# Optimization experiments

Measured on AMD Instinct MI355X. Metric: run time of the kernel, lower is better.

The kernel has to match this reference:

```python
import jax, jax.numpy as jnp
import numpy as np

EPS = 1e-5

def _layernorm(x, g, b):
    mu = jnp.mean(x, axis=-1, keepdims=True)
    var = jnp.mean(jnp.square(x - mu), axis=-1, keepdims=True)
    return (x - mu) * jax.lax.rsqrt(var + EPS) * g + b

def setup_inputs() -> dict:
    key = jax.random.key(0)
    ks = jax.random.split(key, 6)
    B, S, D, F = 32768, 8, 192, 384
    sd = 1.0 / np.sqrt(D)
    return {
        "x": jax.random.normal(ks[0], (B, S, D), jnp.float32),
        "w_qkv": jax.random.normal(ks[1], (D, 3 * D), jnp.float32) * sd,
        "w_out": jax.random.normal(ks[2], (D, D), jnp.float32) * sd,
        "b_out": jnp.zeros((D,), jnp.float32),
        "g1": jnp.ones((D,), jnp.float32),
        "b1": jnp.zeros((D,), jnp.float32),
        "g2": jnp.ones((D,), jnp.float32),
        "b2": jnp.zeros((D,), jnp.float32),
        "w_f1": jax.random.normal(ks[3], (D, F), jnp.float32) * sd,
        "b_f1": jnp.zeros((F,), jnp.float32),
        "w_f2": jax.random.normal(ks[4], (F, D), jnp.float32) * (1.0 / np.sqrt(F)),
        "b_f2": jnp.zeros((D,), jnp.float32),
    }

def reference(x, w_qkv, w_out, b_out, g1, b1, g2, b2, w_f1, b_f1, w_f2, b_f2):
    B, S, D = x.shape
    H = 4
    DH = D // H
    scale = DH ** -0.5
    normed = _layernorm(x, g1, b1)
    qkv = jnp.einsum('bsd,de->bse', normed, w_qkv)  # (B,S,3D)
    q, k, v = jnp.split(qkv, 3, axis=-1)
    q = q.reshape(B, S, H, DH)
    k = k.reshape(B, S, H, DH)
    v = v.reshape(B, S, H, DH)
    attn = jnp.einsum('bqhd,bkhd->bhqk', q, k) * scale
    attn = jax.nn.softmax(attn, axis=-1)
    out = jnp.einsum('bhqk,bkhd->bqhd', attn, v).reshape(B, S, D)
    out = jnp.einsum('bsd,de->bse', out, w_out) + b_out
    x = x + out
    h = _layernorm(x, g2, b2)
    h = jax.nn.gelu(jnp.einsum('bsd,df->bsf', h, w_f1) + b_f1, approximate=False)
    h = jnp.einsum('bsf,fd->bsd', h, w_f2) + b_f2
    return x + h
```

## Files before the change

kernel.cpp:

```cpp
#include <hip/hip_runtime.h>
#include <hip/hip_bf16.h>

typedef __bf16 bf16x8 __attribute__((ext_vector_type(8)));
typedef float f32x4 __attribute__((ext_vector_type(4)));

#define DEV static __device__ __forceinline__

DEV unsigned short f2b(float f) {
  return __builtin_bit_cast(unsigned short, __float2bfloat16(f));
}
DEV unsigned pk2(float a, float b) {
  return (unsigned)f2b(a) | ((unsigned)f2b(b) << 16);
}
DEV void unpack2(unsigned u, float& lo, float& hi) {
  lo = __uint_as_float(u << 16);
  hi = __uint_as_float(u & 0xffff0000u);
}
DEV float gelu_fast(float h) {
  float u = h * (1.5957691216f + 0.0713554f * h * h);
  float e = __expf(u);
  float r = __builtin_amdgcn_rcpf(e + 1.f);
  return h - h * r;
}

__global__ void pack_weights(const float* __restrict__ wq,
                             const float* __restrict__ wo,
                             const float* __restrict__ wf1,
                             const float* __restrict__ wf2,
                             unsigned short* __restrict__ ws) {
  int i = blockIdx.x * 256 + threadIdx.x;
  const float* src; int j, N, KC;
  if (i < 110592)      { j = i;          src = wq;  N = 576; KC = 6; }
  else if (i < 147456) { j = i - 110592; src = wo;  N = 192; KC = 6; }
  else if (i < 221184) { j = i - 147456; src = wf1; N = 384; KC = 6; }
  else                 { j = i - 221184; src = wf2; N = 192; KC = 12; }
  int tk = j >> 9, r = j & 511;
  int nt = tk / KC, kc = tk % KC;
  int n = nt * 16 + (r >> 5), k = kc * 32 + (r & 31);
  ws[i] = f2b(src[k * N + n]);
}

template<int NT, int KC, typename EPI>
DEV void gemm_stage(const unsigned short* As, int astride,
                    const unsigned short* Bp, int nt0, int KCtot,
                    int lr, int kg, EPI epi) {
  bf16x8 af[2][KC];
  #pragma unroll
  for (int m = 0; m < 2; ++m)
    #pragma unroll
    for (int kc = 0; kc < KC; ++kc)
      af[m][kc] = *(const bf16x8*)(As + (m * 16 + lr) * astride + kc * 32 + kg * 8);
  const unsigned short* bb = Bp + lr * 32 + kg * 8;
  bf16x8 bbuf[2][KC];
  #pragma unroll
  for (int kc = 0; kc < KC; ++kc)
    bbuf[0][kc] = *(const bf16x8*)(bb + (size_t)(nt0 * KCtot + kc) * 512);
  #pragma unroll
  for (int nt = 0; nt < NT; ++nt) {
    if (nt + 1 < NT) {
      #pragma unroll
      for (int kc = 0; kc < KC; ++kc)
        bbuf[(nt + 1) & 1][kc] =
            *(const bf16x8*)(bb + (size_t)((nt0 + nt + 1) * KCtot + kc) * 512);
    }
    f32x4 acc[2] = {};
    #pragma unroll
    for (int kc = 0; kc < KC; ++kc)
      #pragma unroll
      for (int m = 0; m < 2; ++m)
        acc[m] = __builtin_amdgcn_mfma_f32_16x16x32_bf16(bbuf[nt & 1][kc], af[m][kc], acc[m], 0, 0, 0);
    epi(nt, acc);
  }
}

template<bool ADD_A>
DEV void layernorm_pass(const float* __restrict__ xg, const unsigned short* Abuf,
                        unsigned short* dst,
                        const float* __restrict__ gg, const float* __restrict__ bb,
                        int t) {
  int r = t >> 3, q = t & 7;
  float vals[24];
  float s = 0.f;
  #pragma unroll
  for (int j = 0; j < 6; ++j) {
    float4 v = *(const float4*)(xg + (size_t)r * 192 + q * 24 + j * 4);
    if (ADD_A) {
      uint2 a2 = *(const uint2*)(Abuf + r * 392 + 192 + q * 24 + j * 4);
      float a0, a1, a2f, a3;
      unpack2(a2.x, a0, a1); unpack2(a2.y, a2f, a3);
      v.x += a0; v.y += a1; v.z += a2f; v.w += a3;
    }
    vals[j*4+0] = v.x; vals[j*4+1] = v.y; vals[j*4+2] = v.z; vals[j*4+3] = v.w;
    s += v.x + v.y + v.z + v.w;
  }
  s += __shfl_xor(s, 1); s += __shfl_xor(s, 2); s += __shfl_xor(s, 4);
  float mu = s * (1.f / 192.f);
  float ss = 0.f;
  #pragma unroll
  for (int i = 0; i < 24; ++i) { float d = vals[i] - mu; ss += d * d; }
  ss += __shfl_xor(ss, 1); ss += __shfl_xor(ss, 2); ss += __shfl_xor(ss, 4);
  float rstd = rsqrtf(ss * (1.f / 192.f) + 1e-5f);
  #pragma unroll
  for (int j = 0; j < 6; ++j) {
    int c = q * 24 + j * 4;
    float4 g4 = *(const float4*)(gg + c);
    float4 b4 = *(const float4*)(bb + c);
    uint2 u;
    u.x = pk2((vals[j*4+0] - mu) * rstd * g4.x + b4.x,
              (vals[j*4+1] - mu) * rstd * g4.y + b4.y);
    u.y = pk2((vals[j*4+2] - mu) * rstd * g4.z + b4.z,
              (vals[j*4+3] - mu) * rstd * g4.w + b4.w);
    *(uint2*)(dst + r * 200 + c) = u;
  }
}

__global__ __launch_bounds__(256, 3)
void fused_block(const float* __restrict__ x,
                 const float* __restrict__ g1, const float* __restrict__ b1,
                 const float* __restrict__ g2, const float* __restrict__ b2,
                 const float* __restrict__ b_out, const float* __restrict__ b_f1,
                 const float* __restrict__ b_f2,
                 const unsigned short* __restrict__ wq_t,
                 const unsigned short* __restrict__ wo_t,
                 const unsigned short* __restrict__ wf1_t,
                 const unsigned short* __restrict__ wf2_t,
                 float* __restrict__ out)
{
  __shared__ __align__(16) unsigned short r1[32 * 200];
  __shared__ __align__(16) unsigned short r2[32 * 392];

  const int t = threadIdx.x;
  const int wave = t >> 6;
  const int lane = t & 63;
  const int lr = lane & 15;
  const int kg = lane >> 4;
  const int token0 = blockIdx.x * 32;
  const float* xg = x + (size_t)token0 * 192;
  float* og = out + (size_t)token0 * 192;

  layernorm_pass<false>(xg, nullptr, r1, g1, b1, t);
  __syncthreads();

  gemm_stage<6, 6>(r1, 200, wq_t, wave * 6, 6, lr, kg,
    [&](int nt, f32x4 (&acc)[2]) {
      int n0 = (wave * 6 + nt) * 16 + kg * 4;
      #pragma unroll
      for (int m = 0; m < 2; ++m) {
        uint2 u; u.x = pk2(acc[m][0], acc[m][1]); u.y = pk2(acc[m][2], acc[m][3]);
        *(uint2*)(r2 + (m * 16 + lr) * 392 + n0) = u;
      }
    });
  __syncthreads();

  const int ag = t >> 4, aqi = (t >> 1) & 7, ahalf = t & 1;
  const int abl = ag >> 2, ah = ag & 3;
  const int aqrow = abl * 8 + aqi;
  const int ad0 = ahalf * 24;
  float p[8];
  {
    float qv[24];
    const uint4* qp = (const uint4*)(r2 + aqrow * 392 + ah * 48 + ad0);
    #pragma unroll
    for (int u = 0; u < 3; ++u) {
      uint4 w4 = qp[u];
      unpack2(w4.x, qv[u*8+0], qv[u*8+1]);
      unpack2(w4.y, qv[u*8+2], qv[u*8+3]);
      unpack2(w4.z, qv[u*8+4], qv[u*8+5]);
      unpack2(w4.w, qv[u*8+6], qv[u*8+7]);
    }
    #pragma unroll
    for (int j = 0; j < 8; ++j) {
      const uint4* kp = (const uint4*)(r2 + (abl * 8 + j) * 392 + 192 + ah * 48 + ad0);
      float d = 0.f;
      #pragma unroll
      for (int u = 0; u < 3; ++u) {
        uint4 w4 = kp[u];
        float lo, hi;
        unpack2(w4.x, lo, hi); d = fmaf(lo, qv[u*8+0], d); d = fmaf(hi, qv[u*8+1], d);
        unpack2(w4.y, lo, hi); d = fmaf(lo, qv[u*8+2], d); d = fmaf(hi, qv[u*8+3], d);
        unpack2(w4.z, lo, hi); d = fmaf(lo, qv[u*8+4], d); d = fmaf(hi, qv[u*8+5], d);
        unpack2(w4.w, lo, hi); d = fmaf(lo, qv[u*8+6], d); d = fmaf(hi, qv[u*8+7], d);
      }
      d += __shfl_xor(d, 1);
      p[j] = d * 0.14433756729740643f;
    }
    float mx = p[0];
    #pragma unroll
    for (int j = 1; j < 8; ++j) mx = fmaxf(mx, p[j]);
    float sum = 0.f;
    #pragma unroll
    for (int j = 0; j < 8; ++j) { p[j] = __expf(p[j] - mx); sum += p[j]; }
    float inv = 1.f / sum;
    #pragma unroll
    for (int j = 0; j < 8; ++j) p[j] *= inv;
  }
  __syncthreads();

  gemm_stage<3, 6>(r1, 200, wq_t, 24 + wave * 3, 6, lr, kg,
    [&](int nt, f32x4 (&acc)[2]) {
      int n0 = (wave * 3 + nt) * 16 + kg * 4;
      #pragma unroll
      for (int m = 0; m < 2; ++m) {
        uint2 u; u.x = pk2(acc[m][0], acc[m][1]); u.y = pk2(acc[m][2], acc[m][3]);
        *(uint2*)(r2 + (m * 16 + lr) * 392 + n0) = u;
      }
    });
  __syncthreads();

  {
    float oa[24];
    #pragma unroll
    for (int e = 0; e < 24; ++e) oa[e] = 0.f;
    #pragma unroll
    for (int j = 0; j < 8; ++j) {
      float pj = p[j];
      const uint4* vp = (const uint4*)(r2 + (abl * 8 + j) * 392 + ah * 48 + ad0);
      #pragma unroll
      for (int u = 0; u < 3; ++u) {
        uint4 w4 = vp[u];
        float lo, hi;
        unpack2(w4.x, lo, hi); oa[u*8+0] = fmaf(pj, lo, oa[u*8+0]); oa[u*8+1] = fmaf(pj, hi, oa[u*8+1]);
        unpack2(w4.y, lo, hi); oa[u*8+2] = fmaf(pj, lo, oa[u*8+2]); oa[u*8+3] = fmaf(pj, hi, oa[u*8+3]);
        unpack2(w4.z, lo, hi); oa[u*8+4] = fmaf(pj, lo, oa[u*8+4]); oa[u*8+5] = fmaf(pj, hi, oa[u*8+5]);
        unpack2(w4.w, lo, hi); oa[u*8+6] = fmaf(pj, lo, oa[u*8+6]); oa[u*8+7] = fmaf(pj, hi, oa[u*8+7]);
      }
    }
    uint4 ov[3];
    #pragma unroll
    for (int u = 0; u < 3; ++u) {
      ov[u].x = pk2(oa[u*8+0], oa[u*8+1]);
      ov[u].y = pk2(oa[u*8+2], oa[u*8+3]);
      ov[u].z = pk2(oa[u*8+4], oa[u*8+5]);
      ov[u].w = pk2(oa[u*8+6], oa[u*8+7]);
    }
    uint4* op = (uint4*)(r1 + aqrow * 200 + ah * 48 + ad0);
    #pragma unroll
    for (int u = 0; u < 3; ++u) op[u] = ov[u];
  }
  __syncthreads();

  uint2 areg[3][2];
  gemm_stage<3, 6>(r1, 200, wo_t, wave * 3, 6, lr, kg,
    [&](int nt, f32x4 (&acc)[2]) {
      int n0 = (wave * 3 + nt) * 16 + kg * 4;
      float4 bo = *(const float4*)(b_out + n0);
      #pragma unroll
      for (int m = 0; m < 2; ++m) {
        uint2 u;
        u.x = pk2(acc[m][0] + bo.x, acc[m][1] + bo.y);
        u.y = pk2(acc[m][2] + bo.z, acc[m][3] + bo.w);
        areg[nt][m] = u;
        *(uint2*)(r2 + (m * 16 + lr) * 392 + 192 + n0) = u;
      }
    });
  __syncthreads();

  layernorm_pass<true>(xg, r2, r1, g2, b2, t);
  __syncthreads();

  gemm_stage<6, 6>(r1, 200, wf1_t, wave * 6, 6, lr, kg,
    [&](int nt, f32x4 (&acc)[2]) {
      int n0 = (wave * 6 + nt) * 16 + kg * 4;
      float4 bf = *(const float4*)(b_f1 + n0);
      #pragma unroll
      for (int m = 0; m < 2; ++m) {
        float ge[4];
        #pragma unroll
        for (int i = 0; i < 4; ++i)
          ge[i] = gelu_fast(acc[m][i] + ((const float*)&bf)[i]);
        uint2 u; u.x = pk2(ge[0], ge[1]); u.y = pk2(ge[2], ge[3]);
        *(uint2*)(r2 + (m * 16 + lr) * 392 + n0) = u;
      }
    });
  __syncthreads();

  {
    f32x4 acc[3][2] = {};
    bf16x8 afb[2][2], bvb[2][3];
    #pragma unroll
    for (int m = 0; m < 2; ++m)
      afb[0][m] = *(const bf16x8*)(r2 + (m * 16 + lr) * 392 + kg * 8);
    #pragma unroll
    for (int nt = 0; nt < 3; ++nt)
      bvb[0][nt] = *(const bf16x8*)(wf2_t + (size_t)((wave * 3 + nt) * 12) * 512 + lr * 32 + kg * 8);
    #pragma unroll
    for (int kc = 0; kc < 12; ++kc) {
      if (kc + 1 < 12) {
        #pragma unroll
        for (int m = 0; m < 2; ++m)
          afb[(kc + 1) & 1][m] =
              *(const bf16x8*)(r2 + (m * 16 + lr) * 392 + (kc + 1) * 32 + kg * 8);
        #pragma unroll
        for (int nt = 0; nt < 3; ++nt)
          bvb[(kc + 1) & 1][nt] =
              *(const bf16x8*)(wf2_t + (size_t)((wave * 3 + nt) * 12 + kc + 1) * 512 + lr * 32 + kg * 8);
      }
      #pragma unroll
      for (int nt = 0; nt < 3; ++nt)
        #pragma unroll
        for (int m = 0; m < 2; ++m)
          acc[nt][m] = __builtin_amdgcn_mfma_f32_16x16x32_bf16(bvb[kc & 1][nt], afb[kc & 1][m], acc[nt][m], 0, 0, 0);
    }
    #pragma unroll
    for (int nt = 0; nt < 3; ++nt) {
      int n0 = (wave * 3 + nt) * 16 + kg * 4;
      float4 bf = *(const float4*)(b_f2 + n0);
      #pragma unroll
      for (int m = 0; m < 2; ++m) {
        int row = m * 16 + lr;
        float4 xv = *(const float4*)(xg + (size_t)row * 192 + n0);
        float a0, a1, a2f, a3;
        unpack2(areg[nt][m].x, a0, a1); unpack2(areg[nt][m].y, a2f, a3);
        float4 o;
        o.x = xv.x + a0  + acc[nt][m][0] + bf.x;
        o.y = xv.y + a1  + acc[nt][m][1] + bf.y;
        o.z = xv.z + a2f + acc[nt][m][2] + bf.z;
        o.w = xv.w + a3  + acc[nt][m][3] + bf.w;
        *(float4*)(og + (size_t)row * 192 + n0) = o;
      }
    }
  }
}

extern "C" void kernel_launch(void* const* d_in, const int* in_sizes, int n_in,
                              void* d_out, int out_size, void* d_ws, size_t ws_size,
                              hipStream_t stream) {
  const float* x   = (const float*)d_in[0];
  const float* wq  = (const float*)d_in[1];
  const float* wo  = (const float*)d_in[2];
  const float* bo  = (const float*)d_in[3];
  const float* g1  = (const float*)d_in[4];
  const float* b1  = (const float*)d_in[5];
  const float* g2  = (const float*)d_in[6];
  const float* b2  = (const float*)d_in[7];
  const float* wf1 = (const float*)d_in[8];
  const float* bf1 = (const float*)d_in[9];
  const float* wf2 = (const float*)d_in[10];
  const float* bf2 = (const float*)d_in[11];
  unsigned short* wsb = (unsigned short*)d_ws;

  pack_weights<<<1152, 256, 0, stream>>>(wq, wo, wf1, wf2, wsb);

  int tokens = in_sizes[0] / 192;
  int nb = tokens / 32;
  fused_block<<<nb, 256, 0, stream>>>(x, g1, b1, g2, b2, bo, bf1, bf2,
      wsb, wsb + 110592, wsb + 147456, wsb + 221184, (float*)d_out);
}
```

Before: 376.6 us.

## Prefetch weight tiles and x rows before barriers; use native bf16 pack

```diff
diff --git a/kernel.cpp b/kernel.cpp
--- a/kernel.cpp
+++ b/kernel.cpp
@@ -2,15 +2,18 @@
 #include <hip/hip_bf16.h>
 
 typedef __bf16 bf16x8 __attribute__((ext_vector_type(8)));
+typedef __bf16 bf16x2 __attribute__((ext_vector_type(2)));
 typedef float f32x4 __attribute__((ext_vector_type(4)));
 
 #define DEV static __device__ __forceinline__
 
 DEV unsigned short f2b(float f) {
-  return __builtin_bit_cast(unsigned short, __float2bfloat16(f));
+  __bf16 h = (__bf16)f;
+  return __builtin_bit_cast(unsigned short, h);
 }
 DEV unsigned pk2(float a, float b) {
-  return (unsigned)f2b(a) | ((unsigned)f2b(b) << 16);
+  bf16x2 v; v[0] = (__bf16)a; v[1] = (__bf16)b;
+  return __builtin_bit_cast(unsigned, v);
 }
 DEV void unpack2(unsigned u, float& lo, float& hi) {
   lo = __uint_as_float(u << 16);
@@ -40,10 +43,19 @@
   ws[i] = f2b(src[k * N + n]);
 }
 
+template<int KC>
+DEV void load_b0(bf16x8 (&dst)[KC], const unsigned short* Bp, int nt0, int KCtot,
+                 int lr, int kg) {
+  const unsigned short* bb = Bp + (size_t)(nt0 * KCtot) * 512 + lr * 32 + kg * 8;
+  #pragma unroll
+  for (int kc = 0; kc < KC; ++kc)
+    dst[kc] = *(const bf16x8*)(bb + kc * 512);
+}
+
 template<int NT, int KC, typename EPI>
 DEV void gemm_stage(const unsigned short* As, int astride,
                     const unsigned short* Bp, int nt0, int KCtot,
-                    int lr, int kg, EPI epi) {
+                    int lr, int kg, const bf16x8 (&b0)[KC], EPI epi) {
   bf16x8 af[2][KC];
   #pragma unroll
   for (int m = 0; m < 2; ++m)
@@ -53,8 +65,7 @@
   const unsigned short* bb = Bp + lr * 32 + kg * 8;
   bf16x8 bbuf[2][KC];
   #pragma unroll
-  for (int kc = 0; kc < KC; ++kc)
-    bbuf[0][kc] = *(const bf16x8*)(bb + (size_t)(nt0 * KCtot + kc) * 512);
+  for (int kc = 0; kc < KC; ++kc) bbuf[0][kc] = b0[kc];
   #pragma unroll
   for (int nt = 0; nt < NT; ++nt) {
     if (nt + 1 < NT) {
@@ -74,7 +85,7 @@
 }
 
 template<bool ADD_A>
-DEV void layernorm_pass(const float* __restrict__ xg, const unsigned short* Abuf,
+DEV void layernorm_pass(const float4 (&xv)[6], const unsigned short* Abuf,
                         unsigned short* dst,
                         const float* __restrict__ gg, const float* __restrict__ bb,
                         int t) {
@@ -83,7 +94,7 @@
   float s = 0.f;
   #pragma unroll
   for (int j = 0; j < 6; ++j) {
-    float4 v = *(const float4*)(xg + (size_t)r * 192 + q * 24 + j * 4);
+    float4 v = xv[j];
     if (ADD_A) {
       uint2 a2 = *(const uint2*)(Abuf + r * 392 + 192 + q * 24 + j * 4);
       float a0, a1, a2f, a3;
@@ -137,11 +148,19 @@
   const int token0 = blockIdx.x * 32;
   const float* xg = x + (size_t)token0 * 192;
   float* og = out + (size_t)token0 * 192;
-
-  layernorm_pass<false>(xg, nullptr, r1, g1, b1, t);
-  __syncthreads();
-
-  gemm_stage<6, 6>(r1, 200, wq_t, wave * 6, 6, lr, kg,
+  const int lnr = t >> 3, lnq = t & 7;
+
+  float4 xv[6];
+  #pragma unroll
+  for (int j = 0; j < 6; ++j)
+    xv[j] = *(const float4*)(xg + (size_t)lnr * 192 + lnq * 24 + j * 4);
+  bf16x8 b0[6];
+  load_b0<6>(b0, wq_t, wave * 6, 6, lr, kg);
+
+  layernorm_pass<false>(xv, nullptr, r1, g1, b1, t);
+  __syncthreads();
+
+  gemm_stage<6, 6>(r1, 200, wq_t, wave * 6, 6, lr, kg, b0,
     [&](int nt, f32x4 (&acc)[2]) {
       int n0 = (wave * 6 + nt) * 16 + kg * 4;
       #pragma unroll
@@ -150,6 +169,8 @@
         *(uint2*)(r2 + (m * 16 + lr) * 392 + n0) = u;
       }
     });
+  bf16x8 b0v[6];
+  load_b0<6>(b0v, wq_t, 24 + wave * 3, 6, lr, kg);
   __syncthreads();
 
   const int ag = t >> 4, aqi = (t >> 1) & 7, ahalf = t & 1;
@@ -196,7 +217,7 @@
   }
   __syncthreads();
 
-  gemm_stage<3, 6>(r1, 200, wq_t, 24 + wave * 3, 6, lr, kg,
+  gemm_stage<3, 6>(r1, 200, wq_t, 24 + wave * 3, 6, lr, kg, b0v,
     [&](int nt, f32x4 (&acc)[2]) {
       int n0 = (wave * 3 + nt) * 16 + kg * 4;
       #pragma unroll
@@ -205,6 +226,8 @@
         *(uint2*)(r2 + (m * 16 + lr) * 392 + n0) = u;
       }
     });
+  bf16x8 b0o[6];
+  load_b0<6>(b0o, wo_t, wave * 3, 6, lr, kg);
   __syncthreads();
 
   {
@@ -240,7 +263,7 @@
   __syncthreads();
 
   uint2 areg[3][2];
-  gemm_stage<3, 6>(r1, 200, wo_t, wave * 3, 6, lr, kg,
+  gemm_stage<3, 6>(r1, 200, wo_t, wave * 3, 6, lr, kg, b0o,
     [&](int nt, f32x4 (&acc)[2]) {
       int n0 = (wave * 3 + nt) * 16 + kg * 4;
       float4 bo = *(const float4*)(b_out + n0);
@@ -253,12 +276,18 @@
         *(uint2*)(r2 + (m * 16 + lr) * 392 + 192 + n0) = u;
       }
     });
-  __syncthreads();
-
-  layernorm_pass<true>(xg, r2, r1, g2, b2, t);
-  __syncthreads();
-
-  gemm_stage<6, 6>(r1, 200, wf1_t, wave * 6, 6, lr, kg,
+  #pragma unroll
+  for (int j = 0; j < 6; ++j)
+    xv[j] = *(const float4*)(xg + (size_t)lnr * 192 + lnq * 24 + j * 4);
+  __syncthreads();
+
+  bf16x8 b0f[6];
+  load_b0<6>(b0f, wf1_t, wave * 6, 6, lr, kg);
+
+  layernorm_pass<true>(xv, r2, r1, g2, b2, t);
+  __syncthreads();
+
+  gemm_stage<6, 6>(r1, 200, wf1_t, wave * 6, 6, lr, kg, b0f,
     [&](int nt, f32x4 (&acc)[2]) {
       int n0 = (wave * 6 + nt) * 16 + kg * 4;
       float4 bf = *(const float4*)(b_f1 + n0);
@@ -272,6 +301,16 @@
         *(uint2*)(r2 + (m * 16 + lr) * 392 + n0) = u;
       }
     });
+  bf16x8 bvb0[3];
+  #pragma unroll
+  for (int nt = 0; nt < 3; ++nt)
+    bvb0[nt] = *(const bf16x8*)(wf2_t + (size_t)((wave * 3 + nt) * 12) * 512 + lr * 32 + kg * 8);
+  float4 xo[3][2];
+  #pragma unroll
+  for (int nt = 0; nt < 3; ++nt)
+    #pragma unroll
+    for (int m = 0; m < 2; ++m)
+      xo[nt][m] = *(const float4*)(xg + (size_t)(m * 16 + lr) * 192 + (wave * 3 + nt) * 16 + kg * 4);
   __syncthreads();
 
   {
@@ -282,7 +321,7 @@
       afb[0][m] = *(const bf16x8*)(r2 + (m * 16 + lr) * 392 + kg * 8);
     #pragma unroll
     for (int nt = 0; nt < 3; ++nt)
-      bvb[0][nt] = *(const bf16x8*)(wf2_t + (size_t)((wave * 3 + nt) * 12) * 512 + lr * 32 + kg * 8);
+      bvb[0][nt] = bvb0[nt];
     #pragma unroll
     for (int kc = 0; kc < 12; ++kc) {
       if (kc + 1 < 12) {
@@ -308,14 +347,14 @@
       #pragma unroll
       for (int m = 0; m < 2; ++m) {
         int row = m * 16 + lr;
-        float4 xv = *(const float4*)(xg + (size_t)row * 192 + n0);
+        float4 xvv = xo[nt][m];
         float a0, a1, a2f, a3;
         unpack2(areg[nt][m].x, a0, a1); unpack2(areg[nt][m].y, a2f, a3);
         float4 o;
-        o.x = xv.x + a0  + acc[nt][m][0] + bf.x;
-        o.y = xv.y + a1  + acc[nt][m][1] + bf.y;
-        o.z = xv.z + a2f + acc[nt][m][2] + bf.z;
-        o.w = xv.w + a3  + acc[nt][m][3] + bf.w;
+        o.x = xvv.x + a0  + acc[nt][m][0] + bf.x;
+        o.y = xvv.y + a1  + acc[nt][m][1] + bf.y;
+        o.z = xvv.z + a2f + acc[nt][m][2] + bf.z;
+        o.w = xvv.w + a3  + acc[nt][m][3] + bf.w;
         *(float4*)(og + (size_t)row * 192 + n0) = o;
       }
     }
```

Result: slower. 622.1 us (+65.2%).

## Triple-buffer weight prefetch and restructure FFN2 GEMM into K-split passes

Applied to the files above, without the earlier changes.

```diff
diff --git a/kernel.cpp b/kernel.cpp
--- a/kernel.cpp
+++ b/kernel.cpp
@@ -2,15 +2,18 @@
 #include <hip/hip_bf16.h>
 
 typedef __bf16 bf16x8 __attribute__((ext_vector_type(8)));
+typedef __bf16 bf16x2 __attribute__((ext_vector_type(2)));
 typedef float f32x4 __attribute__((ext_vector_type(4)));
 
 #define DEV static __device__ __forceinline__
 
 DEV unsigned short f2b(float f) {
-  return __builtin_bit_cast(unsigned short, __float2bfloat16(f));
+  __bf16 h = (__bf16)f;
+  return __builtin_bit_cast(unsigned short, h);
 }
 DEV unsigned pk2(float a, float b) {
-  return (unsigned)f2b(a) | ((unsigned)f2b(b) << 16);
+  bf16x2 v; v[0] = (__bf16)a; v[1] = (__bf16)b;
+  return __builtin_bit_cast(unsigned, v);
 }
 DEV void unpack2(unsigned u, float& lo, float& hi) {
   lo = __uint_as_float(u << 16);
@@ -51,24 +54,29 @@
     for (int kc = 0; kc < KC; ++kc)
       af[m][kc] = *(const bf16x8*)(As + (m * 16 + lr) * astride + kc * 32 + kg * 8);
   const unsigned short* bb = Bp + lr * 32 + kg * 8;
-  bf16x8 bbuf[2][KC];
+  bf16x8 bbuf[3][KC];
   #pragma unroll
   for (int kc = 0; kc < KC; ++kc)
     bbuf[0][kc] = *(const bf16x8*)(bb + (size_t)(nt0 * KCtot + kc) * 512);
+  if (NT > 1) {
+    #pragma unroll
+    for (int kc = 0; kc < KC; ++kc)
+      bbuf[1][kc] = *(const bf16x8*)(bb + (size_t)((nt0 + 1) * KCtot + kc) * 512);
+  }
   #pragma unroll
   for (int nt = 0; nt < NT; ++nt) {
-    if (nt + 1 < NT) {
+    if (nt + 2 < NT) {
       #pragma unroll
       for (int kc = 0; kc < KC; ++kc)
-        bbuf[(nt + 1) & 1][kc] =
-            *(const bf16x8*)(bb + (size_t)((nt0 + nt + 1) * KCtot + kc) * 512);
+        bbuf[(nt + 2) % 3][kc] =
+            *(const bf16x8*)(bb + (size_t)((nt0 + nt + 2) * KCtot + kc) * 512);
     }
     f32x4 acc[2] = {};
     #pragma unroll
     for (int kc = 0; kc < KC; ++kc)
       #pragma unroll
       for (int m = 0; m < 2; ++m)
-        acc[m] = __builtin_amdgcn_mfma_f32_16x16x32_bf16(bbuf[nt & 1][kc], af[m][kc], acc[m], 0, 0, 0);
+        acc[m] = __builtin_amdgcn_mfma_f32_16x16x32_bf16(bbuf[nt % 3][kc], af[m][kc], acc[m], 0, 0, 0);
     epi(nt, acc);
   }
 }
@@ -275,31 +283,34 @@
   __syncthreads();
 
   {
-    f32x4 acc[3][2] = {};
-    bf16x8 afb[2][2], bvb[2][3];
-    #pragma unroll
-    for (int m = 0; m < 2; ++m)
-      afb[0][m] = *(const bf16x8*)(r2 + (m * 16 + lr) * 392 + kg * 8);
-    #pragma unroll
-    for (int nt = 0; nt < 3; ++nt)
-      bvb[0][nt] = *(const bf16x8*)(wf2_t + (size_t)((wave * 3 + nt) * 12) * 512 + lr * 32 + kg * 8);
-    #pragma unroll
-    for (int kc = 0; kc < 12; ++kc) {
-      if (kc + 1 < 12) {
+    f32x4 acc4[3][2] = {};
+    #pragma unroll
+    for (int pass = 0; pass < 2; ++pass) {
+      bf16x8 af[2][6];
+      #pragma unroll
+      for (int m = 0; m < 2; ++m)
         #pragma unroll
-        for (int m = 0; m < 2; ++m)
-          afb[(kc + 1) & 1][m] =
-              *(const bf16x8*)(r2 + (m * 16 + lr) * 392 + (kc + 1) * 32 + kg * 8);
+        for (int kc = 0; kc < 6; ++kc)
+          af[m][kc] = *(const bf16x8*)(r2 + (m * 16 + lr) * 392 + (pass * 6 + kc) * 32 + kg * 8);
+      const unsigned short* bb = wf2_t + lr * 32 + kg * 8;
+      bf16x8 bbuf[2][6];
+      #pragma unroll
+      for (int kc = 0; kc < 6; ++kc)
+        bbuf[0][kc] = *(const bf16x8*)(bb + (size_t)((wave * 3 + 0) * 12 + pass * 6 + kc) * 512);
+      #pragma unroll
+      for (int nt = 0; nt < 3; ++nt) {
+        if (nt + 1 < 3) {
+          #pragma unroll
+          for (int kc = 0; kc < 6; ++kc)
+            bbuf[(nt + 1) & 1][kc] =
+                *(const bf16x8*)(bb + (size_t)((wave * 3 + nt + 1) * 12 + pass * 6 + kc) * 512);
+        }
         #pragma unroll
-        for (int nt = 0; nt < 3; ++nt)
-          bvb[(kc + 1) & 1][nt] =
-              *(const bf16x8*)(wf2_t + (size_t)((wave * 3 + nt) * 12 + kc + 1) * 512 + lr * 32 + kg * 8);
-      }
-      #pragma unroll
-      for (int nt = 0; nt < 3; ++nt)
-        #pragma unroll
-        for (int m = 0; m < 2; ++m)
-          acc[nt][m] = __builtin_amdgcn_mfma_f32_16x16x32_bf16(bvb[kc & 1][nt], afb[kc & 1][m], acc[nt][m], 0, 0, 0);
+        for (int kc = 0; kc < 6; ++kc)
+          #pragma unroll
+          for (int m = 0; m < 2; ++m)
+            acc4[nt][m] = __builtin_amdgcn_mfma_f32_16x16x32_bf16(bbuf[nt & 1][kc], af[m][kc], acc4[nt][m], 0, 0, 0);
+      }
     }
     #pragma unroll
     for (int nt = 0; nt < 3; ++nt) {
@@ -312,10 +323,10 @@
         float a0, a1, a2f, a3;
         unpack2(areg[nt][m].x, a0, a1); unpack2(areg[nt][m].y, a2f, a3);
         float4 o;
-        o.x = xv.x + a0  + acc[nt][m][0] + bf.x;
-        o.y = xv.y + a1  + acc[nt][m][1] + bf.y;
-        o.z = xv.z + a2f + acc[nt][m][2] + bf.z;
-        o.w = xv.w + a3  + acc[nt][m][3] + bf.w;
+        o.x = xv.x + a0  + acc4[nt][m][0] + bf.x;
+        o.y = xv.y + a1  + acc4[nt][m][1] + bf.y;
+        o.z = xv.z + a2f + acc4[nt][m][2] + bf.z;
+        o.w = xv.w + a3  + acc4[nt][m][3] + bf.w;
         *(float4*)(og + (size_t)row * 192 + n0) = o;
       }
     }
```

After: 581.6 us. 1.54x slower.
